# Performance work log

Measured on AMD Instinct MI355X. Metric: run time of the kernel, lower is better.

## Reference

```python
import jax, jax.numpy as jnp
import numpy as np

N = 100000   # nodes
E = 1600000  # edges
F = 128      # node features
H = 64       # hidden_dim
G = 64       # graphs in batch


def setup_inputs() -> dict:
    key = jax.random.key(0)
    ks = jax.random.split(key, 12)
    x = jax.random.normal(ks[0], (N, F), jnp.float32)
    edge_index = jax.random.randint(ks[1], (2, E), 0, N, dtype=jnp.int64)
    batch = jnp.sort(jax.random.randint(ks[2], (N,), 0, G, dtype=jnp.int64))
    s = 0.05
    W1 = jax.random.normal(ks[3], (F, H), jnp.float32) * s
    b1 = jnp.zeros((H,), jnp.float32)
    W2 = jax.random.normal(ks[4], (H, H), jnp.float32) * s
    b2 = jnp.zeros((H,), jnp.float32)
    Wa = jax.random.normal(ks[5], (H, 1), jnp.float32) * s
    ba = jnp.zeros((1,), jnp.float32)
    Wc = jax.random.normal(ks[6], (H, 1), jnp.float32) * s
    bc = jnp.zeros((1,), jnp.float32)
    return {"x": x, "edge_index": edge_index, "batch": batch,
            "W1": W1, "b1": b1, "W2": W2, "b2": b2,
            "Wa": Wa, "ba": ba, "Wc": Wc, "bc": bc}


def _gcn_norm(edge_index, n):
    # Add self-loops, compute symmetric normalization deg^-1/2[src]*deg^-1/2[dst]
    loop = jnp.arange(n, dtype=edge_index.dtype)
    src = jnp.concatenate([edge_index[0], loop])
    dst = jnp.concatenate([edge_index[1], loop])
    deg = jax.ops.segment_sum(jnp.ones_like(src, jnp.float32), dst, num_segments=n)
    dinv = jnp.where(deg > 0, deg ** -0.5, 0.0)
    norm = dinv[src] * dinv[dst]  # [E+N]
    return src, dst, norm


def _gcn_conv(x, W, b, src, dst, norm, n):
    h = x @ W                         # [n, H] dense transform first (PyG order)
    msg = h[src] * norm[:, None]      # gather + normalize [E+n, H]
    agg = jax.ops.segment_sum(msg, dst, num_segments=n)  # scatter-add
    return agg + b


def reference(x, edge_index, batch, W1, b1, W2, b2, Wa, ba, Wc, bc):
    n = x.shape[0]
    src, dst, norm = _gcn_norm(edge_index, n)
    h = jax.nn.relu(_gcn_conv(x, W1, b1, src, dst, norm, n))
    # dropout p=0.1 is identity in eval mode
    h = jax.nn.relu(_gcn_conv(h, W2, b2, src, dst, norm, n))
    action_logits = (h @ Wa + ba)[:, 0]  # [N]
    counts = jax.ops.segment_sum(jnp.ones((n,), jnp.float32), batch, num_segments=G)
    pooled = jax.ops.segment_sum(h, batch, num_segments=G) / jnp.maximum(counts, 1.0)[:, None]
    value = pooled @ Wc + bc  # [G, 1]
    return action_logits, value
```

## Files before the change

kernel.cpp:

```cpp
#include <hip/hip_runtime.h>
#include <hip/hip_fp16.h>
#include <math.h>

#define FEAT 128
#define HID  64
#define BSH  7
#define BNODES (1 << BSH)
#define PB   256
#define SRCM ((1u << 25) - 1)


__global__ void part_hist_k(const int* __restrict__ dst, int* __restrict__ table,
                            int e, int nb) {
    __shared__ int lcnt[1024];
    for (int i = threadIdx.x; i < nb; i += 256) lcnt[i] = 0;
    __syncthreads();
    int eb = (e + PB - 1) / PB;
    int lo = blockIdx.x * eb, hi = min(lo + eb, e);
    for (int i = lo + threadIdx.x; i < hi; i += 256)
        atomicAdd(&lcnt[dst[i] >> BSH], 1);
    __syncthreads();
    for (int k = threadIdx.x; k < nb; k += 256)
        table[k * PB + blockIdx.x] = lcnt[k];
}

__global__ void scan1_k(int* __restrict__ data, int* __restrict__ aux, int L) {
    __shared__ int s[1024];
    int gid = blockIdx.x * 1024 + threadIdx.x;
    int v = (gid < L) ? data[gid] : 0;
    s[threadIdx.x] = v;
    __syncthreads();
    for (int off = 1; off < 1024; off <<= 1) {
        int t = (threadIdx.x >= off) ? s[threadIdx.x - off] : 0;
        __syncthreads();
        s[threadIdx.x] += t;
        __syncthreads();
    }
    if (gid < L) data[gid] = s[threadIdx.x] - v;
    if (threadIdx.x == 1023) aux[blockIdx.x] = s[1023];
}

__global__ void scan2_k(int* aux, int naux) {
    __shared__ int s[1024];
    int v = (threadIdx.x < naux) ? aux[threadIdx.x] : 0;
    s[threadIdx.x] = v;
    __syncthreads();
    for (int off = 1; off < 1024; off <<= 1) {
        int t = (threadIdx.x >= off) ? s[threadIdx.x - off] : 0;
        __syncthreads();
        s[threadIdx.x] += t;
        __syncthreads();
    }
    if (threadIdx.x < naux) aux[threadIdx.x] = s[threadIdx.x] - v;
}

__global__ void part_scatter_k(const int* __restrict__ src, const int* __restrict__ dst,
                               const int* __restrict__ table, const int* __restrict__ aux,
                               unsigned* __restrict__ packed, int e, int nb) {
    __shared__ int loff[1024];
    for (int k = threadIdx.x; k < nb; k += 256) {
        int idx = k * PB + blockIdx.x;
        loff[k] = table[idx] + aux[idx >> 10];
    }
    __syncthreads();
    int eb = (e + PB - 1) / PB;
    int lo = blockIdx.x * eb, hi = min(lo + eb, e);
    for (int i = lo + threadIdx.x; i < hi; i += 256) {
        int d = dst[i];
        int p = atomicAdd(&loff[d >> BSH], 1);
        packed[p] = ((unsigned)(d & (BNODES - 1)) << 25) | (unsigned)src[i];
    }
}


__global__ void bucket_sort_k(const unsigned* __restrict__ packed,
                              const int* __restrict__ table, const int* __restrict__ aux,
                              int* __restrict__ col, int* __restrict__ rowptr,
                              float* __restrict__ dinv, int n, int e, int nb) {
    __shared__ int cnt[BNODES];
    __shared__ int s[BNODES];
    __shared__ int cur[BNODES];
    const int k = blockIdx.x;
    const int t = threadIdx.x;
    if (t < BNODES) cnt[t] = 0;
    __syncthreads();
    int i0 = k * PB;
    int i1 = (k + 1) * PB;
    const int bs = table[i0] + aux[i0 >> 10];
    const int be = (k + 1 < nb) ? (table[i1] + aux[i1 >> 10]) : e;
    for (int i = bs + t; i < be; i += 256)
        atomicAdd(&cnt[packed[i] >> 25], 1);
    __syncthreads();
    if (t < BNODES) s[t] = cnt[t];
    __syncthreads();
    for (int off = 1; off < BNODES; off <<= 1) {
        int v = (t < BNODES && t >= off) ? s[t - off] : 0;
        __syncthreads();
        if (t < BNODES) s[t] += v;
        __syncthreads();
    }
    if (t < BNODES) {
        int base = bs + s[t] - cnt[t];
        cur[t] = base;
        int node = (k << BSH) + t;
        if (node < n) {
            rowptr[node] = base;
            dinv[node] = 1.0f / sqrtf(1.0f + (float)cnt[t]);
            if (node == n - 1) rowptr[n] = base + cnt[t];
        }
    }
    __syncthreads();
    for (int i = bs + t; i < be; i += 256) {
        unsigned u = packed[i];
        int p = atomicAdd(&cur[u >> 25], 1);
        col[p] = (int)(u & SRCM);
    }
}


template<int K, bool IN16>
__global__ __launch_bounds__(256, (K == 128) ? 3 : 4)
void gemm_tile_k(const void* __restrict__ Xv, const float* __restrict__ W,
                 const float* __restrict__ dinv, __half* __restrict__ out, int n) {
    __shared__ float sX[64][K + 4];
    __shared__ float sW[64][64];
    const int row0 = blockIdx.x * 64;
    const int t  = threadIdx.x;
    const int tx = t & 15;
    const int ty = t >> 4;
    constexpr int KSH = (K == 128) ? 7 : 6;

    if constexpr (!IN16) {
        const float* xb = (const float*)Xv + (size_t)row0 * K;
#pragma unroll
        for (int it = 0; it < K / 16; ++it) {
            int fl = it * 1024 + t * 4;
            int r  = fl >> KSH;
            int k  = fl & (K - 1);
            float4 v = make_float4(0.f, 0.f, 0.f, 0.f);
            if (row0 + r < n) v = *(const float4*)(xb + fl);
            *(float4*)&sX[r][k] = v;
        }
    } else {
        const __half* xb = (const __half*)Xv + (size_t)row0 * K;
#pragma unroll
        for (int it = 0; it < K / 32; ++it) {
            int fl = it * 2048 + t * 8;
            int r  = fl >> KSH;
            int k  = fl & (K - 1);
            float4 raw = make_float4(0.f, 0.f, 0.f, 0.f);
            if (row0 + r < n) raw = *(const float4*)(xb + fl);
            const __half2* hp = (const __half2*)&raw;
#pragma unroll
            for (int j = 0; j < 4; ++j) {
                float2 f = __half22float2(hp[j]);
                sX[r][k + 2 * j]     = f.x;
                sX[r][k + 2 * j + 1] = f.y;
            }
        }
    }

    float acc[4][4] = {};
#pragma unroll
    for (int ph = 0; ph < K / 64; ++ph) {
        __syncthreads();
#pragma unroll
        for (int it = 0; it < 4; ++it) {
            int fl = it * 1024 + t * 4;
            *(float4*)&sW[fl >> 6][fl & 63] = *(const float4*)(W + ph * 64 * HID + fl);
        }
        __syncthreads();

#pragma unroll 8
        for (int k = 0; k < 64; k += 4) {
            float4 a[4], b[4];
#pragma unroll
            for (int i = 0; i < 4; i++) a[i] = *(float4*)&sX[ty * 4 + i][ph * 64 + k];
#pragma unroll
            for (int j = 0; j < 4; j++) b[j] = *(float4*)&sW[k + j][tx * 4];
#pragma unroll
            for (int i = 0; i < 4; i++) {
                acc[i][0] = fmaf(a[i].x, b[0].x, acc[i][0]);
                acc[i][1] = fmaf(a[i].x, b[0].y, acc[i][1]);
                acc[i][2] = fmaf(a[i].x, b[0].z, acc[i][2]);
                acc[i][3] = fmaf(a[i].x, b[0].w, acc[i][3]);
                acc[i][0] = fmaf(a[i].y, b[1].x, acc[i][0]);
                acc[i][1] = fmaf(a[i].y, b[1].y, acc[i][1]);
                acc[i][2] = fmaf(a[i].y, b[1].z, acc[i][2]);
                acc[i][3] = fmaf(a[i].y, b[1].w, acc[i][3]);
                acc[i][0] = fmaf(a[i].z, b[2].x, acc[i][0]);
                acc[i][1] = fmaf(a[i].z, b[2].y, acc[i][1]);
                acc[i][2] = fmaf(a[i].z, b[2].z, acc[i][2]);
                acc[i][3] = fmaf(a[i].z, b[2].w, acc[i][3]);
                acc[i][0] = fmaf(a[i].w, b[3].x, acc[i][0]);
                acc[i][1] = fmaf(a[i].w, b[3].y, acc[i][1]);
                acc[i][2] = fmaf(a[i].w, b[3].z, acc[i][2]);
                acc[i][3] = fmaf(a[i].w, b[3].w, acc[i][3]);
            }
        }
    }

#pragma unroll
    for (int i = 0; i < 4; i++) {
        int gr = row0 + ty * 4 + i;
        if (gr < n) {
            float sc = dinv[gr];
            union { __half2 h[2]; unsigned long long u; } pk;
            pk.h[0] = __floats2half2_rn(acc[i][0] * sc, acc[i][1] * sc);
            pk.h[1] = __floats2half2_rn(acc[i][2] * sc, acc[i][3] * sc);
            *(unsigned long long*)(out + (size_t)gr * HID + tx * 4) = pk.u;
        }
    }
}


template<bool LOGITS>
__global__ void gather_k(const __half* __restrict__ tS, const int* __restrict__ rowptr,
                         const int* __restrict__ col, const float* __restrict__ dinv,
                         const float* __restrict__ b, __half* __restrict__ out,
                         const float* __restrict__ Wa, const float* __restrict__ ba,
                         float* __restrict__ logits, const int* __restrict__ batch,
                         float* __restrict__ pooled, int n) {
    __shared__ float pga[8][64];
    __shared__ int   garr[8];
    int node = (int)((blockIdx.x * (size_t)blockDim.x + threadIdx.x) >> 5);
    int lane = threadIdx.x & 31;
    int w    = threadIdx.x >> 5;
    bool active = node < n;
    if (!LOGITS && !active) return;

    float h0 = 0.f, h1 = 0.f;
    if (active) {
        int beg = rowptr[node], end = rowptr[node + 1];
        const __half2* tl = (const __half2*)tS + lane;
        float2 acc = __half22float2(tl[node * 32]);
        int e = beg;
        for (; e + 16 <= end; e += 16) {
            int s[16];
            __half2 v[16];
#pragma unroll
            for (int j = 0; j < 16; j++) s[j] = col[e + j];
#pragma unroll
            for (int j = 0; j < 16; j++) v[j] = tl[s[j] * 32];
            float2 t0 = make_float2(0.f, 0.f), t1 = make_float2(0.f, 0.f);
#pragma unroll
            for (int j = 0; j < 8; j++) {
                float2 f = __half22float2(v[j]);
                t0.x += f.x; t0.y += f.y;
            }
#pragma unroll
            for (int j = 8; j < 16; j++) {
                float2 f = __half22float2(v[j]);
                t1.x += f.x; t1.y += f.y;
            }
            acc.x += t0.x + t1.x;
            acc.y += t0.y + t1.y;
        }
        for (; e + 4 <= end; e += 4) {
            __half2 v0 = tl[col[e] * 32];
            __half2 v1 = tl[col[e + 1] * 32];
            __half2 v2 = tl[col[e + 2] * 32];
            __half2 v3 = tl[col[e + 3] * 32];
            float2 f0 = __half22float2(v0), f1 = __half22float2(v1);
            float2 f2 = __half22float2(v2), f3 = __half22float2(v3);
            acc.x += (f0.x + f1.x) + (f2.x + f3.x);
            acc.y += (f0.y + f1.y) + (f2.y + f3.y);
        }
        for (; e < end; ++e) {
            float2 f = __half22float2(tl[col[e] * 32]);
            acc.x += f.x; acc.y += f.y;
        }
        float d = dinv[node];
        float2 bb = *(const float2*)(b + 2 * lane);
        h0 = fmaxf(fmaf(d, acc.x, bb.x), 0.0f);
        h1 = fmaxf(fmaf(d, acc.y, bb.y), 0.0f);
        if (!LOGITS) {
            ((__half2*)out)[node * 32 + lane] = __floats2half2_rn(h0, h1);
        } else {
            float2 wa = *(const float2*)(Wa + 2 * lane);
            float p = h0 * wa.x + h1 * wa.y;
#pragma unroll
            for (int off = 16; off > 0; off >>= 1) p += __shfl_down(p, off, 32);
            if (lane == 0) logits[node] = p + ba[0];
        }
    }

    if (LOGITS) {
        *(float2*)&pga[w][2 * lane] = make_float2(active ? h0 : 0.f, active ? h1 : 0.f);
        if (lane == 0) garr[w] = active ? batch[node] : 0x7fffffff;
        __syncthreads();
        int g0 = garr[0];
        bool uniform = true;
#pragma unroll
        for (int i = 1; i < 8; i++) uniform &= (garr[i] == g0 || garr[i] == 0x7fffffff);
        if (uniform) {
            if (threadIdx.x < 64) {
                float s = 0.f;
#pragma unroll
                for (int i = 0; i < 8; i++) s += pga[i][threadIdx.x];
                atomicAdd(&pooled[g0 * HID + threadIdx.x], s);
            }
        } else if (active) {
            int gg = garr[w];
            atomicAdd(&pooled[gg * HID + 2 * lane], h0);
            atomicAdd(&pooled[gg * HID + 2 * lane + 1], h1);
        }
    }
}


__global__ void value_k(const float* __restrict__ pooled, const int* __restrict__ batch,
                        const float* __restrict__ Wc, const float* __restrict__ bc,
                        float* __restrict__ val, int n, int g) {
    int gw   = (int)((blockIdx.x * (size_t)blockDim.x + threadIdx.x) >> 6);
    int lane = threadIdx.x & 63;
    if (gw >= g) return;
    int lo = 0, hi = n;
    while (lo < hi) { int m = (lo + hi) >> 1; if (batch[m] < gw) lo = m + 1; else hi = m; }
    int b0 = lo;
    lo = 0; hi = n;
    while (lo < hi) { int m = (lo + hi) >> 1; if (batch[m] < gw + 1) lo = m + 1; else hi = m; }
    float cnt = fmaxf((float)(lo - b0), 1.0f);
    float p = (pooled[gw * HID + lane] / cnt) * Wc[lane];
#pragma unroll
    for (int off = 32; off > 0; off >>= 1) p += __shfl_down(p, off);
    if (lane == 0) val[gw] = p + bc[0];
}

extern "C" void kernel_launch(void* const* d_in, const int* in_sizes, int n_in,
                              void* d_out, int out_size, void* d_ws, size_t ws_size,
                              hipStream_t stream) {
    const float* x     = (const float*)d_in[0];
    const int*   ei    = (const int*)d_in[1];
    const int*   batch = (const int*)d_in[2];
    const float* W1    = (const float*)d_in[3];
    const float* b1    = (const float*)d_in[4];
    const float* W2    = (const float*)d_in[5];
    const float* b2    = (const float*)d_in[6];
    const float* Wa    = (const float*)d_in[7];
    const float* ba    = (const float*)d_in[8];
    const float* Wc    = (const float*)d_in[9];
    const float* bc    = (const float*)d_in[10];

    const int n = in_sizes[0] / FEAT;
    const int e = in_sizes[1] / 2;
    const int g = out_size - n;
    const int* src = ei;
    const int* dst = ei + e;

    const int nb = (n + BNODES - 1) >> BSH;
    const int L  = nb * PB;

    float*    ws     = (float*)d_ws;
    float*    dinv   = ws;
    float*    bufA   = dinv + n;
    float*    bufB   = bufA + (size_t)n * HID;
    float*    pooled = bufB + (size_t)n * HID;
    int*      table  = (int*)(pooled + (size_t)g * HID);
    int*      aux    = table + L;
    int*      rowptr = aux + 1024;
    int*      col    = rowptr + n + 1;
    unsigned* packed = (unsigned*)bufA;
    __half*   tS     = (__half*)bufA;
    __half*   h16    = (__half*)bufB;

    const int B = 256;
    const int gridT = (n + 63) / 64;
    const int gridG = (int)(((size_t)n * 32 + B - 1) / B);
    const int nb1   = (L + 1023) / 1024;

    hipMemsetAsync(pooled, 0, (size_t)g * HID * sizeof(float), stream);

    part_hist_k<<<PB, B, 0, stream>>>(dst, table, e, nb);
    scan1_k<<<nb1, 1024, 0, stream>>>(table, aux, L);
    scan2_k<<<1, 1024, 0, stream>>>(aux, nb1);
    part_scatter_k<<<PB, B, 0, stream>>>(src, dst, table, aux, packed, e, nb);
    bucket_sort_k<<<nb, B, 0, stream>>>(packed, table, aux, col, rowptr, dinv, n, e, nb);

    gemm_tile_k<FEAT, false><<<gridT, B, 0, stream>>>(x, W1, dinv, tS, n);
    gather_k<false><<<gridG, B, 0, stream>>>(tS, rowptr, col, dinv, b1, h16,
                                             nullptr, nullptr, nullptr, nullptr, nullptr, n);

    gemm_tile_k<HID, true><<<gridT, B, 0, stream>>>(h16, W2, dinv, tS, n);
    gather_k<true><<<gridG, B, 0, stream>>>(tS, rowptr, col, dinv, b2, nullptr,
                                            Wa, ba, (float*)d_out, batch, pooled, n);

    value_k<<<(g * 64 + B - 1) / B, B, 0, stream>>>(pooled, batch, Wc, bc,
                                                    (float*)d_out + n, n, g);
}
```

Baseline: 304.4 us.

## Split hidden features into 4 planes for gather locality and separate pooling

Stores the fp16 hidden features in four planes of 16 features each, so every gather block handles one plane for 32 nodes with 8 lanes per node. The intent is to shrink the working set of each gather pass so random neighbour reads hit L2/MALL more often. Logits are now built by atomic adds across slices, which needs a memset of the output, and mean pooling moves into a new pool_k kernel that reads the stored layer-2 features. This adds an extra write of the hidden features, an extra kernel launch and atomics on the logits.

```diff
diff --git a/kernel.cpp b/kernel.cpp
--- a/kernel.cpp
+++ b/kernel.cpp
@@ -8,6 +8,7 @@
 #define BNODES (1 << BSH)
 #define PB   256
 #define SRCM ((1u << 25) - 1)
+#define SL   4
 
 
 __global__ void part_hist_k(const int* __restrict__ dst, int* __restrict__ table,
@@ -142,14 +143,17 @@
             *(float4*)&sX[r][k] = v;
         }
     } else {
-        const __half* xb = (const __half*)Xv + (size_t)row0 * K;
+        const __half* xb = (const __half*)Xv;
 #pragma unroll
         for (int it = 0; it < K / 32; ++it) {
             int fl = it * 2048 + t * 8;
-            int r  = fl >> KSH;
-            int k  = fl & (K - 1);
+            int r  = fl >> 6;
+            int k  = fl & 63;
+            int plane = k >> 4;
+            int off   = k & 15;
             float4 raw = make_float4(0.f, 0.f, 0.f, 0.f);
-            if (row0 + r < n) raw = *(const float4*)(xb + fl);
+            if (row0 + r < n)
+                raw = *(const float4*)(xb + ((size_t)plane * n + row0 + r) * 16 + off);
             const __half2* hp = (const __half2*)&raw;
 #pragma unroll
             for (int j = 0; j < 4; ++j) {
@@ -208,7 +212,8 @@
             union { __half2 h[2]; unsigned long long u; } pk;
             pk.h[0] = __floats2half2_rn(acc[i][0] * sc, acc[i][1] * sc);
             pk.h[1] = __floats2half2_rn(acc[i][2] * sc, acc[i][3] * sc);
-            *(unsigned long long*)(out + (size_t)gr * HID + tx * 4) = pk.u;
+            __half* pl = out + ((size_t)(tx >> 2) * n + gr) * 16 + (tx & 3) * 4;
+            *(unsigned long long*)pl = pk.u;
         }
     }
 }
@@ -219,93 +224,99 @@
                          const int* __restrict__ col, const float* __restrict__ dinv,
                          const float* __restrict__ b, __half* __restrict__ out,
                          const float* __restrict__ Wa, const float* __restrict__ ba,
-                         float* __restrict__ logits, const int* __restrict__ batch,
-                         float* __restrict__ pooled, int n) {
-    __shared__ float pga[8][64];
-    __shared__ int   garr[8];
-    int node = (int)((blockIdx.x * (size_t)blockDim.x + threadIdx.x) >> 5);
-    int lane = threadIdx.x & 31;
-    int w    = threadIdx.x >> 5;
-    bool active = node < n;
-    if (!LOGITS && !active) return;
-
-    float h0 = 0.f, h1 = 0.f;
-    if (active) {
-        int beg = rowptr[node], end = rowptr[node + 1];
-        const __half2* tl = (const __half2*)tS + lane;
-        float2 acc = __half22float2(tl[node * 32]);
-        int e = beg;
-        for (; e + 16 <= end; e += 16) {
-            int s[16];
-            __half2 v[16];
-#pragma unroll
-            for (int j = 0; j < 16; j++) s[j] = col[e + j];
-#pragma unroll
-            for (int j = 0; j < 16; j++) v[j] = tl[s[j] * 32];
-            float2 t0 = make_float2(0.f, 0.f), t1 = make_float2(0.f, 0.f);
-#pragma unroll
-            for (int j = 0; j < 8; j++) {
-                float2 f = __half22float2(v[j]);
-                t0.x += f.x; t0.y += f.y;
+                         float* __restrict__ logits, int n) {
+    const int slice = blockIdx.x & (SL - 1);
+    const int chunk = blockIdx.x >> 2;
+    const int nl = threadIdx.x >> 3;
+    const int l8 = threadIdx.x & 7;
+    const int node = chunk * 32 + nl;
+    if (node >= n) return;
+    const int fp = slice * 8 + l8;
+
+    int beg = rowptr[node], end = rowptr[node + 1];
+    const __half2* tp = (const __half2*)tS + (size_t)slice * n * 8 + l8;
+    float2 acc = __half22float2(tp[node * 8]);
+    int e = beg;
+    for (; e + 16 <= end; e += 16) {
+        int s[16];
+        __half2 v[16];
+#pragma unroll
+        for (int j = 0; j < 16; j++) s[j] = __builtin_nontemporal_load(col + e + j);
+#pragma unroll
+        for (int j = 0; j < 16; j++) v[j] = tp[s[j] * 8];
+        float2 t0 = make_float2(0.f, 0.f), t1 = make_float2(0.f, 0.f);
+#pragma unroll
+        for (int j = 0; j < 8; j++) {
+            float2 f = __half22float2(v[j]);
+            t0.x += f.x; t0.y += f.y;
+        }
+#pragma unroll
+        for (int j = 8; j < 16; j++) {
+            float2 f = __half22float2(v[j]);
+            t1.x += f.x; t1.y += f.y;
+        }
+        acc.x += t0.x + t1.x;
+        acc.y += t0.y + t1.y;
+    }
+    for (; e + 4 <= end; e += 4) {
+        __half2 v0 = tp[col[e] * 8];
+        __half2 v1 = tp[col[e + 1] * 8];
+        __half2 v2 = tp[col[e + 2] * 8];
+        __half2 v3 = tp[col[e + 3] * 8];
+        float2 f0 = __half22float2(v0), f1 = __half22float2(v1);
+        float2 f2 = __half22float2(v2), f3 = __half22float2(v3);
+        acc.x += (f0.x + f1.x) + (f2.x + f3.x);
+        acc.y += (f0.y + f1.y) + (f2.y + f3.y);
+    }
+    for (; e < end; ++e) {
+        float2 f = __half22float2(tp[col[e] * 8]);
+        acc.x += f.x; acc.y += f.y;
+    }
+    float d = dinv[node];
+    float2 bb = *(const float2*)(b + 2 * fp);
+    float h0 = fmaxf(fmaf(d, acc.x, bb.x), 0.0f);
+    float h1 = fmaxf(fmaf(d, acc.y, bb.y), 0.0f);
+    __half2 hv = __floats2half2_rn(h0, h1);
+    unsigned int* op = (unsigned int*)((__half2*)out + (size_t)slice * n * 8 + node * 8 + l8);
+    union { __half2 h; unsigned int u; } cv; cv.h = hv;
+    __builtin_nontemporal_store(cv.u, op);
+    if (LOGITS) {
+        float2 wa = *(const float2*)(Wa + 2 * fp);
+        float p = h0 * wa.x + h1 * wa.y;
+        p += __shfl_down(p, 4, 8);
+        p += __shfl_down(p, 2, 8);
+        p += __shfl_down(p, 1, 8);
+        if (l8 == 0) atomicAdd(&logits[node], p + (slice == 0 ? ba[0] : 0.0f));
+    }
+}
+
+
+__global__ void pool_k(const __half* __restrict__ h, const int* __restrict__ batch,
+                       float* __restrict__ pooled, int n) {
+    const int slice = blockIdx.x & (SL - 1);
+    const int grp = (blockIdx.x >> 2) * 32 + (threadIdx.x >> 3);
+    const int l8 = threadIdx.x & 7;
+    int start = grp * 32;
+    if (start >= n) return;
+    int end = min(start + 32, n);
+    const __half2* hp = (const __half2*)h + (size_t)slice * n * 8 + l8;
+    const int fbase = 2 * (slice * 8 + l8);
+    float2 acc = make_float2(0.f, 0.f);
+    int curg = -1;
+    for (int i = start; i < end; i++) {
+        int g = batch[i];
+        if (g != curg) {
+            if (curg >= 0) {
+                atomicAdd(&pooled[curg * HID + fbase], acc.x);
+                atomicAdd(&pooled[curg * HID + fbase + 1], acc.y);
             }
-#pragma unroll
-            for (int j = 8; j < 16; j++) {
-                float2 f = __half22float2(v[j]);
-                t1.x += f.x; t1.y += f.y;
-            }
-            acc.x += t0.x + t1.x;
-            acc.y += t0.y + t1.y;
-        }
-        for (; e + 4 <= end; e += 4) {
-            __half2 v0 = tl[col[e] * 32];
-            __half2 v1 = tl[col[e + 1] * 32];
-            __half2 v2 = tl[col[e + 2] * 32];
-            __half2 v3 = tl[col[e + 3] * 32];
-            float2 f0 = __half22float2(v0), f1 = __half22float2(v1);
-            float2 f2 = __half22float2(v2), f3 = __half22float2(v3);
-            acc.x += (f0.x + f1.x) + (f2.x + f3.x);
-            acc.y += (f0.y + f1.y) + (f2.y + f3.y);
-        }
-        for (; e < end; ++e) {
-            float2 f = __half22float2(tl[col[e] * 32]);
-            acc.x += f.x; acc.y += f.y;
-        }
-        float d = dinv[node];
-        float2 bb = *(const float2*)(b + 2 * lane);
-        h0 = fmaxf(fmaf(d, acc.x, bb.x), 0.0f);
-        h1 = fmaxf(fmaf(d, acc.y, bb.y), 0.0f);
-        if (!LOGITS) {
-            ((__half2*)out)[node * 32 + lane] = __floats2half2_rn(h0, h1);
-        } else {
-            float2 wa = *(const float2*)(Wa + 2 * lane);
-            float p = h0 * wa.x + h1 * wa.y;
-#pragma unroll
-            for (int off = 16; off > 0; off >>= 1) p += __shfl_down(p, off, 32);
-            if (lane == 0) logits[node] = p + ba[0];
-        }
-    }
-
-    if (LOGITS) {
-        *(float2*)&pga[w][2 * lane] = make_float2(active ? h0 : 0.f, active ? h1 : 0.f);
-        if (lane == 0) garr[w] = active ? batch[node] : 0x7fffffff;
-        __syncthreads();
-        int g0 = garr[0];
-        bool uniform = true;
-#pragma unroll
-        for (int i = 1; i < 8; i++) uniform &= (garr[i] == g0 || garr[i] == 0x7fffffff);
-        if (uniform) {
-            if (threadIdx.x < 64) {
-                float s = 0.f;
-#pragma unroll
-                for (int i = 0; i < 8; i++) s += pga[i][threadIdx.x];
-                atomicAdd(&pooled[g0 * HID + threadIdx.x], s);
-            }
-        } else if (active) {
-            int gg = garr[w];
-            atomicAdd(&pooled[gg * HID + 2 * lane], h0);
-            atomicAdd(&pooled[gg * HID + 2 * lane + 1], h1);
-        }
-    }
+            curg = g; acc = make_float2(0.f, 0.f);
+        }
+        float2 f = __half22float2(hp[i * 8]);
+        acc.x += f.x; acc.y += f.y;
+    }
+    atomicAdd(&pooled[curg * HID + fbase], acc.x);
+    atomicAdd(&pooled[curg * HID + fbase + 1], acc.y);
 }
 
 
@@ -366,10 +377,12 @@
 
     const int B = 256;
     const int gridT = (n + 63) / 64;
-    const int gridG = (int)(((size_t)n * 32 + B - 1) / B);
+    const int gridG = ((n + 31) / 32) * SL;
+    const int gridP = ((n + 32 * 32 - 1) / (32 * 32)) * SL;
     const int nb1   = (L + 1023) / 1024;
 
     hipMemsetAsync(pooled, 0, (size_t)g * HID * sizeof(float), stream);
+    hipMemsetAsync(d_out, 0, (size_t)n * sizeof(float), stream);
 
     part_hist_k<<<PB, B, 0, stream>>>(dst, table, e, nb);
     scan1_k<<<nb1, 1024, 0, stream>>>(table, aux, L);
@@ -379,12 +392,13 @@
 
     gemm_tile_k<FEAT, false><<<gridT, B, 0, stream>>>(x, W1, dinv, tS, n);
     gather_k<false><<<gridG, B, 0, stream>>>(tS, rowptr, col, dinv, b1, h16,
-                                             nullptr, nullptr, nullptr, nullptr, nullptr, n);
+                                             nullptr, nullptr, nullptr, n);
 
     gemm_tile_k<HID, true><<<gridT, B, 0, stream>>>(h16, W2, dinv, tS, n);
-    gather_k<true><<<gridG, B, 0, stream>>>(tS, rowptr, col, dinv, b2, nullptr,
-                                            Wa, ba, (float*)d_out, batch, pooled, n);
-
+    gather_k<true><<<gridG, B, 0, stream>>>(tS, rowptr, col, dinv, b2, (__half*)bufB,
+                                            Wa, ba, (float*)d_out, n);
+
+    pool_k<<<gridP, B, 0, stream>>>((__half*)bufB, batch, pooled, n);
     value_k<<<(g * 64 + B - 1) / B, B, 0, stream>>>(pooled, batch, Wc, bc,
                                                     (float*)d_out + n, n, g);
 }
```

Measured after the change: 355.5 us. +16.8%, slower.
